# Optimization experiments

Hardware: AMD Instinct MI355X
Metric: run time of the kernel (lower is better)

Reference implementation:

```python
import jax, jax.numpy as jnp
import numpy as np

N = 50000
E = 800000
IN_DIM = 256
HID = 256
OUT_DIM = 2


def setup_inputs() -> dict:
    key = jax.random.key(0)
    ks = jax.random.split(key, 10)
    x = jax.random.normal(ks[0], (N, IN_DIM), dtype=jnp.float32)
    edge_index = jax.random.randint(ks[1], (2, E), 0, N, dtype=jnp.int64)
    # Glorot-ish scaling so activations stay well-conditioned through 4 layers
    def w(k, fan_in, fan_out):
        return jax.random.normal(k, (fan_in, fan_out), dtype=jnp.float32) / jnp.sqrt(jnp.float32(fan_in))
    return {
        "x": x,
        "edge_index": edge_index,
        "W0": w(ks[2], IN_DIM, HID), "b0": jnp.zeros((HID,), jnp.float32),
        "W1": w(ks[3], HID, HID),    "b1": jnp.zeros((HID,), jnp.float32),
        "W2": w(ks[4], HID, HID),    "b2": jnp.zeros((HID,), jnp.float32),
        "W3": w(ks[5], HID, OUT_DIM), "b3": jnp.zeros((OUT_DIM,), jnp.float32),
    }


def _gcn_norm(edge_index, n, dtype):
    # PyG gcn_norm with self-loops: deg over destination, norm = d^-1/2[src]*d^-1/2[dst]
    loops = jnp.arange(n, dtype=edge_index.dtype)
    src = jnp.concatenate([edge_index[0], loops])
    dst = jnp.concatenate([edge_index[1], loops])
    deg = jax.ops.segment_sum(jnp.ones_like(dst, dtype=dtype), dst, num_segments=n)
    dis = deg ** -0.5  # deg >= 1 due to self-loops
    norm = dis[src] * dis[dst]
    return src, dst, norm


def reference(x, edge_index, W0, b0, W1, b1, W2, b2, W3, b3):
    n = x.shape[0]
    src, dst, norm = _gcn_norm(edge_index, n, x.dtype)

    def conv(h, W, b):
        h = h @ W                              # [N, F_out] dense GEMM
        msg = h[src] * norm[:, None]           # edge-gather + scale
        agg = jax.ops.segment_sum(msg, dst, num_segments=n)  # scatter-add
        return agg + b

    h = jax.nn.relu(conv(x, W0, b0))
    h = jax.nn.relu(conv(h, W1, b1))
    h = jax.nn.relu(conv(h, W2, b2))
    return conv(h, W3, b3)
```

## Files before the change

kernel.cpp:

```cpp
#include <hip/hip_runtime.h>

#define N_NODES 50000
#define N_EDGES 800000

static inline int cdiv(int a, int b) { return (a + b - 1) / b; }

typedef __attribute__((ext_vector_type(8))) short bf16x8;
typedef __attribute__((ext_vector_type(4))) float f32x4;

static __device__ __forceinline__ unsigned short f2bf(float f) {
    unsigned int u = __float_as_uint(f);
    unsigned int r = (u + 0x7FFF + ((u >> 16) & 1)) >> 16;
    return (unsigned short)r;
}
static __device__ __forceinline__ float bf2f(unsigned short h) {
    return __uint_as_float((unsigned int)h << 16);
}
static __device__ __forceinline__ float bf_lo(unsigned int u) { return __uint_as_float(u << 16); }
static __device__ __forceinline__ float bf_hi(unsigned int u) { return __uint_as_float(u & 0xFFFF0000u); }


__global__ void k_init_cnt(int* cnt, int n) {
    int i = blockIdx.x * 256 + threadIdx.x;
    if (i < n) cnt[i] = 1;
}

__global__ void k_count(const int* __restrict__ edst, int* cnt, int e) {
    int i = blockIdx.x * 256 + threadIdx.x;
    if (i < e) atomicAdd(&cnt[edst[i]], 1);
}

__global__ __launch_bounds__(256) void k_scan1(const int* __restrict__ cnt,
                                               int* __restrict__ row_ptr,
                                               float* __restrict__ dis,
                                               int* __restrict__ blk, int n) {
    __shared__ int sums[256];
    int t = threadIdx.x;
    int base = blockIdx.x * 1024 + t * 4;
    int c0 = 0, c1 = 0, c2 = 0, c3 = 0;
    if (base + 3 < n) {
        int4 v = *(const int4*)(cnt + base);
        c0 = v.x; c1 = v.y; c2 = v.z; c3 = v.w;
    } else {
        if (base + 0 < n) c0 = cnt[base + 0];
        if (base + 1 < n) c1 = cnt[base + 1];
        if (base + 2 < n) c2 = cnt[base + 2];
        if (base + 3 < n) c3 = cnt[base + 3];
    }
    int s = c0 + c1 + c2 + c3;
    sums[t] = s;
    __syncthreads();
    int x = s;
    for (int off = 1; off < 256; off <<= 1) {
        int y = (t >= off) ? sums[t - off] : 0;
        __syncthreads();
        x += y;
        sums[t] = x;
        __syncthreads();
    }
    int excl = x - s;
    if (base + 0 < n) { row_ptr[base + 0] = excl;                dis[base + 0] = rsqrtf((float)c0); }
    if (base + 1 < n) { row_ptr[base + 1] = excl + c0;           dis[base + 1] = rsqrtf((float)c1); }
    if (base + 2 < n) { row_ptr[base + 2] = excl + c0 + c1;      dis[base + 2] = rsqrtf((float)c2); }
    if (base + 3 < n) { row_ptr[base + 3] = excl + c0 + c1 + c2; dis[base + 3] = rsqrtf((float)c3); }
    if (t == 255) blk[blockIdx.x] = x;
}

__global__ __launch_bounds__(256) void k_scan2(int* __restrict__ blk,
                                               int* __restrict__ row_ptr_n, int nb) {
    __shared__ int sums[256];
    int t = threadIdx.x;
    int s = (t < nb) ? blk[t] : 0;
    sums[t] = s;
    __syncthreads();
    int x = s;
    for (int off = 1; off < 256; off <<= 1) {
        int y = (t >= off) ? sums[t - off] : 0;
        __syncthreads();
        x += y;
        sums[t] = x;
        __syncthreads();
    }
    if (t < nb) blk[t] = x - s;
    if (t == 255) row_ptr_n[0] = x;
}

__global__ __launch_bounds__(256) void k_scan3(int* __restrict__ row_ptr,
                                               int* __restrict__ pos,
                                               const int* __restrict__ blk, int n) {
    int base = blockIdx.x * 1024 + threadIdx.x * 4;
    int off = blk[blockIdx.x];
#pragma unroll
    for (int i = 0; i < 4; ++i) {
        int idx = base + i;
        if (idx < n) {
            int v = row_ptr[idx] + off;
            row_ptr[idx] = v;
            pos[idx] = v;
        }
    }
}

__global__ void k_fill_self(int* pos, const float* __restrict__ dis,
                            int* src_s, float* norm_s, int n) {
    int i = blockIdx.x * 256 + threadIdx.x;
    if (i < n) {
        int p = atomicAdd(&pos[i], 1);
        src_s[p] = i;
        float d = dis[i];
        norm_s[p] = d * d;
    }
}

__global__ void k_fill_edges(const int* __restrict__ esrc, const int* __restrict__ edst,
                             int* pos, const float* __restrict__ dis,
                             int* src_s, float* norm_s, int e) {
    int i = blockIdx.x * 256 + threadIdx.x;
    if (i < e) {
        int s = esrc[i], d = edst[i];
        int p = atomicAdd(&pos[d], 1);
        src_s[p] = s;
        norm_s[p] = dis[s] * dis[d];
    }
}


__global__ __launch_bounds__(256) void k_split_w(const float* __restrict__ W,
                                                 unsigned short* __restrict__ Wth,
                                                 unsigned short* __restrict__ Wtl) {
    int n = blockIdx.x;
    int k = threadIdx.x;
    float v = W[(size_t)k * 256 + n];
    unsigned short h = f2bf(v);
    Wth[(size_t)n * 256 + k] = h;
    Wtl[(size_t)n * 256 + k] = f2bf(v - bf2f(h));
}


__global__ __launch_bounds__(256) void k_split_a(const float* __restrict__ X,
                                                 unsigned short* __restrict__ Xh,
                                                 unsigned short* __restrict__ Xl, long total4) {
    long i = (long)blockIdx.x * 256 + threadIdx.x;
    if (i >= total4) return;
    float4 v = *(const float4*)(X + i * 4);
    ushort4 h, l;
    h.x = f2bf(v.x); l.x = f2bf(v.x - bf2f(h.x));
    h.y = f2bf(v.y); l.y = f2bf(v.y - bf2f(h.y));
    h.z = f2bf(v.z); l.z = f2bf(v.z - bf2f(h.z));
    h.w = f2bf(v.w); l.w = f2bf(v.w - bf2f(h.w));
    *(ushort4*)(Xh + i * 4) = h;
    *(ushort4*)(Xl + i * 4) = l;
}


#define GEMM_RB 196

__global__ __launch_bounds__(256) void k_gemm_mfma(const unsigned short* __restrict__ Ah,
                                                   const unsigned short* __restrict__ Al,
                                                   const unsigned short* __restrict__ Wth,
                                                   const unsigned short* __restrict__ Wtl,
                                                   unsigned short* __restrict__ C, int M) {
    __shared__ unsigned short Wh[64][264];
    __shared__ unsigned short Wl[64][264];
    int rowblk = blockIdx.x % GEMM_RB;
    int colblk = blockIdx.x / GEMM_RB;
    int c0 = colblk * 64;
    int m0 = rowblk * 256;
    int t = threadIdx.x;

    {
        int r = t >> 2;
        int k0 = (t & 3) * 64;
        const unsigned short* gh = Wth + (size_t)(c0 + r) * 256 + k0;
        const unsigned short* gl = Wtl + (size_t)(c0 + r) * 256 + k0;
        unsigned short* lh = &Wh[r][k0];
        unsigned short* ll = &Wl[r][k0];
#pragma unroll
        for (int i = 0; i < 8; ++i) {
            *(uint4*)(lh + i * 8) = *(const uint4*)(gh + i * 8);
            *(uint4*)(ll + i * 8) = *(const uint4*)(gl + i * 8);
        }
    }
    __syncthreads();

    int lane = t & 63, wave = t >> 6;
    int quad = lane >> 4, l16 = lane & 15;

    f32x4 acc[4][4];
#pragma unroll
    for (int i = 0; i < 4; ++i)
#pragma unroll
        for (int j = 0; j < 4; ++j) acc[i][j] = (f32x4){0.f, 0.f, 0.f, 0.f};

    for (int kc = 0; kc < 8; ++kc) {
        int ko = kc * 32 + quad * 8;
        bf16x8 ahf[4], alf[4];
#pragma unroll
        for (int mt = 0; mt < 4; ++mt) {
            int m = m0 + wave * 64 + mt * 16 + l16;
            if (m >= M) m = M - 1;
            ahf[mt] = *(const bf16x8*)(Ah + (size_t)m * 256 + ko);
            alf[mt] = *(const bf16x8*)(Al + (size_t)m * 256 + ko);
        }
#pragma unroll
        for (int nt = 0; nt < 4; ++nt) {
            bf16x8 bh = *(const bf16x8*)&Wh[nt * 16 + l16][ko];
            bf16x8 bl = *(const bf16x8*)&Wl[nt * 16 + l16][ko];
#pragma unroll
            for (int mt = 0; mt < 4; ++mt) {
                acc[mt][nt] = __builtin_amdgcn_mfma_f32_16x16x32_bf16(ahf[mt], bh, acc[mt][nt], 0, 0, 0);
                acc[mt][nt] = __builtin_amdgcn_mfma_f32_16x16x32_bf16(ahf[mt], bl, acc[mt][nt], 0, 0, 0);
                acc[mt][nt] = __builtin_amdgcn_mfma_f32_16x16x32_bf16(alf[mt], bh, acc[mt][nt], 0, 0, 0);
            }
        }
    }

#pragma unroll
    for (int mt = 0; mt < 4; ++mt) {
#pragma unroll
        for (int r = 0; r < 4; ++r) {
            int row = m0 + wave * 64 + mt * 16 + quad * 4 + r;
            if (row < M) {
                unsigned short* cp = C + (size_t)row * 256 + c0 + l16;
#pragma unroll
                for (int nt = 0; nt < 4; ++nt) cp[nt * 16] = f2bf(acc[mt][nt][r]);
            }
        }
    }
}


__global__ __launch_bounds__(256) void k_agg256(const unsigned short* __restrict__ t,
                                                const int* __restrict__ row_ptr,
                                                const int* __restrict__ src_s,
                                                const float* __restrict__ norm_s,
                                                const float* __restrict__ bias,
                                                unsigned short* __restrict__ outh,
                                                unsigned short* __restrict__ outl, int n) {
    int lane = threadIdx.x & 63;
    int wave = threadIdx.x >> 6;
    int node = blockIdx.x * 4 + wave;
    if (node >= n) return;
    int half = lane >> 5;
    int fl = lane & 31;
    int beg = row_ptr[node], end = row_ptr[node + 1];
    float acc[8] = {};
    const unsigned short* tp = t + fl * 8;

    int e = beg + half;
    for (; e + 2 < end; e += 4) {
        int s0 = src_s[e], s1 = src_s[e + 2];
        float w0 = norm_s[e], w1 = norm_s[e + 2];
        uint4 v0 = *(const uint4*)(tp + (size_t)s0 * 256);
        uint4 v1 = *(const uint4*)(tp + (size_t)s1 * 256);
        acc[0] += w0 * bf_lo(v0.x) + w1 * bf_lo(v1.x);
        acc[1] += w0 * bf_hi(v0.x) + w1 * bf_hi(v1.x);
        acc[2] += w0 * bf_lo(v0.y) + w1 * bf_lo(v1.y);
        acc[3] += w0 * bf_hi(v0.y) + w1 * bf_hi(v1.y);
        acc[4] += w0 * bf_lo(v0.z) + w1 * bf_lo(v1.z);
        acc[5] += w0 * bf_hi(v0.z) + w1 * bf_hi(v1.z);
        acc[6] += w0 * bf_lo(v0.w) + w1 * bf_lo(v1.w);
        acc[7] += w0 * bf_hi(v0.w) + w1 * bf_hi(v1.w);
    }
    if (e < end) {
        int s0 = src_s[e];
        float w0 = norm_s[e];
        uint4 v0 = *(const uint4*)(tp + (size_t)s0 * 256);
        acc[0] += w0 * bf_lo(v0.x);
        acc[1] += w0 * bf_hi(v0.x);
        acc[2] += w0 * bf_lo(v0.y);
        acc[3] += w0 * bf_hi(v0.y);
        acc[4] += w0 * bf_lo(v0.z);
        acc[5] += w0 * bf_hi(v0.z);
        acc[6] += w0 * bf_lo(v0.w);
        acc[7] += w0 * bf_hi(v0.w);
    }
#pragma unroll
    for (int i = 0; i < 8; ++i) acc[i] += __shfl_xor(acc[i], 32);

    if (half == 0) {
        const float* bp = bias + fl * 8;
        ushort4 h0, h1, l0, l1;
        float v;
        unsigned short h;
#define EMIT(idx, dst_h, dst_l)                         \
        v = acc[idx] + bp[idx];                         \
        v = v > 0.f ? v : 0.f;                          \
        h = f2bf(v); dst_h = h; dst_l = f2bf(v - bf2f(h));
        EMIT(0, h0.x, l0.x) EMIT(1, h0.y, l0.y) EMIT(2, h0.z, l0.z) EMIT(3, h0.w, l0.w)
        EMIT(4, h1.x, l1.x) EMIT(5, h1.y, l1.y) EMIT(6, h1.z, l1.z) EMIT(7, h1.w, l1.w)
#undef EMIT
        unsigned short* oh = outh + (size_t)node * 256 + fl * 8;
        unsigned short* ol = outl + (size_t)node * 256 + fl * 8;
        *(ushort4*)(oh + 0) = h0;
        *(ushort4*)(oh + 4) = h1;
        *(ushort4*)(ol + 0) = l0;
        *(ushort4*)(ol + 4) = l1;
    }
}


__global__ __launch_bounds__(256) void k_gemm_out2(const unsigned short* __restrict__ Hh,
                                                   const unsigned short* __restrict__ Hl,
                                                   const float* __restrict__ W3,
                                                   float* __restrict__ t2, int n) {
    int lane = threadIdx.x & 63;
    int wave = threadIdx.x >> 6;
    int row = blockIdx.x * 4 + wave;
    if (row >= n) return;
    ushort4 ah = *(const ushort4*)(Hh + (size_t)row * 256 + lane * 4);
    ushort4 al = *(const ushort4*)(Hl + (size_t)row * 256 + lane * 4);
    float4 v;
    v.x = bf2f(ah.x) + bf2f(al.x);
    v.y = bf2f(ah.y) + bf2f(al.y);
    v.z = bf2f(ah.z) + bf2f(al.z);
    v.w = bf2f(ah.w) + bf2f(al.w);
    float4 w01 = *(const float4*)(W3 + lane * 8);
    float4 w23 = *(const float4*)(W3 + lane * 8 + 4);
    float s0 = v.x * w01.x + v.y * w01.z + v.z * w23.x + v.w * w23.z;
    float s1 = v.x * w01.y + v.y * w01.w + v.z * w23.y + v.w * w23.w;
#pragma unroll
    for (int off = 32; off > 0; off >>= 1) {
        s0 += __shfl_down(s0, off);
        s1 += __shfl_down(s1, off);
    }
    if (lane == 0) {
        t2[(size_t)row * 2 + 0] = s0;
        t2[(size_t)row * 2 + 1] = s1;
    }
}

__global__ void k_agg2(const float* __restrict__ t2,
                       const int* __restrict__ row_ptr,
                       const int* __restrict__ src_s,
                       const float* __restrict__ norm_s,
                       const float* __restrict__ b3,
                       float* __restrict__ out, int n) {
    int node = blockIdx.x * 256 + threadIdx.x;
    if (node >= n) return;
    int beg = row_ptr[node], end = row_ptr[node + 1];
    float a0 = 0.f, a1 = 0.f;
    for (int e = beg; e < end; ++e) {
        int s = src_s[e];
        float w = norm_s[e];
        float2 v = *(const float2*)(t2 + (size_t)s * 2);
        a0 += w * v.x;
        a1 += w * v.y;
    }
    out[(size_t)node * 2 + 0] = a0 + b3[0];
    out[(size_t)node * 2 + 1] = a1 + b3[1];
}


extern "C" void kernel_launch(void* const* d_in, const int* in_sizes, int n_in,
                              void* d_out, int out_size, void* d_ws, size_t ws_size,
                              hipStream_t stream) {
    const int N = N_NODES, E = N_EDGES;
    const float* x  = (const float*)d_in[0];
    const int* ei   = (const int*)d_in[1];
    const int* esrc = ei;
    const int* edst = ei + E;
    const float* W0 = (const float*)d_in[2];
    const float* b0 = (const float*)d_in[3];
    const float* W1 = (const float*)d_in[4];
    const float* b1 = (const float*)d_in[5];
    const float* W2 = (const float*)d_in[6];
    const float* b2 = (const float*)d_in[7];
    const float* W3 = (const float*)d_in[8];
    const float* b3 = (const float*)d_in[9];
    float* out = (float*)d_out;

    unsigned short* Ahh = (unsigned short*)d_ws;
    unsigned short* All = Ahh + (size_t)N * 256;
    unsigned short* Tb  = All + (size_t)N * 256;
    unsigned short* Wth = Tb + (size_t)N * 256;
    unsigned short* Wtl = Wth + 256 * 256;
    float* t2     = (float*)(Wtl + 256 * 256);
    float* dis    = t2 + (size_t)N * 2;
    float* norm_s = dis + N;
    int*   cnt    = (int*)(norm_s + (E + N));
    int*   row_ptr= cnt + N;
    int*   pos    = row_ptr + (N + 1);
    int*   src_s  = pos + N;
    int*   blk    = src_s + (E + N);

    const int NB = cdiv(N, 1024);

    k_init_cnt<<<cdiv(N, 256), 256, 0, stream>>>(cnt, N);
    k_count<<<cdiv(E, 256), 256, 0, stream>>>(edst, cnt, E);
    k_scan1<<<NB, 256, 0, stream>>>(cnt, row_ptr, dis, blk, N);
    k_scan2<<<1, 256, 0, stream>>>(blk, row_ptr + N, NB);
    k_scan3<<<NB, 256, 0, stream>>>(row_ptr, pos, blk, N);
    k_fill_self<<<cdiv(N, 256), 256, 0, stream>>>(pos, dis, src_s, norm_s, N);
    k_fill_edges<<<cdiv(E, 256), 256, 0, stream>>>(esrc, edst, pos, dis, src_s, norm_s, E);

    const int ggrid = GEMM_RB * 4;
    const int agrid = cdiv(N, 4);
    const long total4 = (long)N * 64;

    k_split_a<<<cdiv((int)total4, 256), 256, 0, stream>>>(x, Ahh, All, total4);
    k_split_w<<<256, 256, 0, stream>>>(W0, Wth, Wtl);
    k_gemm_mfma<<<ggrid, 256, 0, stream>>>(Ahh, All, Wth, Wtl, Tb, N);
    k_agg256<<<agrid, 256, 0, stream>>>(Tb, row_ptr, src_s, norm_s, b0, Ahh, All, N);
    k_split_w<<<256, 256, 0, stream>>>(W1, Wth, Wtl);
    k_gemm_mfma<<<ggrid, 256, 0, stream>>>(Ahh, All, Wth, Wtl, Tb, N);
    k_agg256<<<agrid, 256, 0, stream>>>(Tb, row_ptr, src_s, norm_s, b1, Ahh, All, N);
    k_split_w<<<256, 256, 0, stream>>>(W2, Wth, Wtl);
    k_gemm_mfma<<<ggrid, 256, 0, stream>>>(Ahh, All, Wth, Wtl, Tb, N);
    k_agg256<<<agrid, 256, 0, stream>>>(Tb, row_ptr, src_s, norm_s, b2, Ahh, All, N);
    k_gemm_out2<<<agrid, 256, 0, stream>>>(Ahh, All, W3, t2, N);
    k_agg2<<<cdiv(N, 256), 256, 0, stream>>>(t2, row_ptr, src_s, norm_s, b3, out, N);
}
```

Measured before the change: 564.8 us.

## Permute hidden feature layout for vector GEMM stores, merge weight-split and fill kernels

The GEMM epilogue now writes four adjacent bf16 outputs as one ushort4 store. To keep this correct, hidden features are stored in a permuted column order, and the weight split, aggregation bias indexing and output GEMM weight indexing are adjusted to match. All three hidden weight splits are merged into one launch with separate buffers, and the self-loop and edge fill kernels are merged into one. Aggregation adds an 8-edge unrolled loop for more memory-level parallelism. The permutation has to stay consistent across layers, and layer 0 keeps the natural input order, which adds index arithmetic.

```diff
diff --git a/kernel.cpp b/kernel.cpp
--- a/kernel.cpp
+++ b/kernel.cpp
@@ -18,6 +18,18 @@
 }
 static __device__ __forceinline__ float bf_lo(unsigned int u) { return __uint_as_float(u << 16); }
 static __device__ __forceinline__ float bf_hi(unsigned int u) { return __uint_as_float(u & 0xFFFF0000u); }
+
+
+static __device__ __forceinline__ void acc8(float* acc, uint4 v, float wgt) {
+    acc[0] += wgt * bf_lo(v.x);
+    acc[1] += wgt * bf_hi(v.x);
+    acc[2] += wgt * bf_lo(v.y);
+    acc[3] += wgt * bf_hi(v.y);
+    acc[4] += wgt * bf_lo(v.z);
+    acc[5] += wgt * bf_hi(v.z);
+    acc[6] += wgt * bf_lo(v.w);
+    acc[7] += wgt * bf_hi(v.w);
+}
 
 
 __global__ void k_init_cnt(int* cnt, int n) {
@@ -101,39 +113,44 @@
     }
 }
 
-__global__ void k_fill_self(int* pos, const float* __restrict__ dis,
-                            int* src_s, float* norm_s, int n) {
-    int i = blockIdx.x * 256 + threadIdx.x;
-    if (i < n) {
-        int p = atomicAdd(&pos[i], 1);
-        src_s[p] = i;
-        float d = dis[i];
-        norm_s[p] = d * d;
-    }
-}
-
-__global__ void k_fill_edges(const int* __restrict__ esrc, const int* __restrict__ edst,
-                             int* pos, const float* __restrict__ dis,
-                             int* src_s, float* norm_s, int e) {
+__global__ void k_fill(const int* __restrict__ esrc, const int* __restrict__ edst,
+                       int* pos, const float* __restrict__ dis,
+                       int* src_s, float* norm_s, int e, int n) {
     int i = blockIdx.x * 256 + threadIdx.x;
     if (i < e) {
         int s = esrc[i], d = edst[i];
         int p = atomicAdd(&pos[d], 1);
         src_s[p] = s;
         norm_s[p] = dis[s] * dis[d];
-    }
-}
-
-
-__global__ __launch_bounds__(256) void k_split_w(const float* __restrict__ W,
-                                                 unsigned short* __restrict__ Wth,
-                                                 unsigned short* __restrict__ Wtl) {
-    int n = blockIdx.x;
-    int k = threadIdx.x;
+    } else if (i < e + n) {
+        int v = i - e;
+        int p = atomicAdd(&pos[v], 1);
+        src_s[p] = v;
+        float d = dis[v];
+        norm_s[p] = d * d;
+    }
+}
+
+
+__global__ __launch_bounds__(256) void k_split_w3(const float* __restrict__ W0,
+                                                  const float* __restrict__ W1,
+                                                  const float* __restrict__ W2,
+                                                  unsigned short* __restrict__ Wth,
+                                                  unsigned short* __restrict__ Wtl) {
+    int layer = blockIdx.x >> 8;
+    int n = blockIdx.x & 255;
+    int p = threadIdx.x;
+    const float* W = layer == 0 ? W0 : (layer == 1 ? W1 : W2);
+    int k = p;
+    if (layer != 0) {
+        int pl = p & 63;
+        k = (p & ~63) + (pl & 3) * 16 + (pl >> 2);
+    }
     float v = W[(size_t)k * 256 + n];
     unsigned short h = f2bf(v);
-    Wth[(size_t)n * 256 + k] = h;
-    Wtl[(size_t)n * 256 + k] = f2bf(v - bf2f(h));
+    size_t o = (size_t)layer * 65536 + (size_t)n * 256 + p;
+    Wth[o] = h;
+    Wtl[o] = f2bf(v - bf2f(h));
 }
 
 
@@ -186,21 +203,30 @@
     int lane = t & 63, wave = t >> 6;
     int quad = lane >> 4, l16 = lane & 15;
 
+    const unsigned short* aph[4];
+    const unsigned short* apl[4];
+#pragma unroll
+    for (int mt = 0; mt < 4; ++mt) {
+        int m = m0 + wave * 64 + mt * 16 + l16;
+        if (m >= M) m = M - 1;
+        aph[mt] = Ah + (size_t)m * 256;
+        apl[mt] = Al + (size_t)m * 256;
+    }
+
     f32x4 acc[4][4];
 #pragma unroll
     for (int i = 0; i < 4; ++i)
 #pragma unroll
         for (int j = 0; j < 4; ++j) acc[i][j] = (f32x4){0.f, 0.f, 0.f, 0.f};
 
+#pragma unroll 2
     for (int kc = 0; kc < 8; ++kc) {
         int ko = kc * 32 + quad * 8;
         bf16x8 ahf[4], alf[4];
 #pragma unroll
         for (int mt = 0; mt < 4; ++mt) {
-            int m = m0 + wave * 64 + mt * 16 + l16;
-            if (m >= M) m = M - 1;
-            ahf[mt] = *(const bf16x8*)(Ah + (size_t)m * 256 + ko);
-            alf[mt] = *(const bf16x8*)(Al + (size_t)m * 256 + ko);
+            ahf[mt] = *(const bf16x8*)(aph[mt] + ko);
+            alf[mt] = *(const bf16x8*)(apl[mt] + ko);
         }
 #pragma unroll
         for (int nt = 0; nt < 4; ++nt) {
@@ -221,9 +247,12 @@
         for (int r = 0; r < 4; ++r) {
             int row = m0 + wave * 64 + mt * 16 + quad * 4 + r;
             if (row < M) {
-                unsigned short* cp = C + (size_t)row * 256 + c0 + l16;
-#pragma unroll
-                for (int nt = 0; nt < 4; ++nt) cp[nt * 16] = f2bf(acc[mt][nt][r]);
+                ushort4 sv;
+                sv.x = f2bf(acc[mt][0][r]);
+                sv.y = f2bf(acc[mt][1][r]);
+                sv.z = f2bf(acc[mt][2][r]);
+                sv.w = f2bf(acc[mt][3][r]);
+                *(ushort4*)(C + (size_t)row * 256 + c0 + l16 * 4) = sv;
             }
         }
     }
@@ -248,48 +277,50 @@
     const unsigned short* tp = t + fl * 8;
 
     int e = beg + half;
+    for (; e + 6 < end; e += 8) {
+        int s0 = src_s[e], s1 = src_s[e + 2], s2 = src_s[e + 4], s3 = src_s[e + 6];
+        float w0 = norm_s[e], w1 = norm_s[e + 2], w2 = norm_s[e + 4], w3 = norm_s[e + 6];
+        uint4 v0 = *(const uint4*)(tp + (size_t)s0 * 256);
+        uint4 v1 = *(const uint4*)(tp + (size_t)s1 * 256);
+        uint4 v2 = *(const uint4*)(tp + (size_t)s2 * 256);
+        uint4 v3 = *(const uint4*)(tp + (size_t)s3 * 256);
+        acc8(acc, v0, w0); acc8(acc, v1, w1); acc8(acc, v2, w2); acc8(acc, v3, w3);
+    }
     for (; e + 2 < end; e += 4) {
         int s0 = src_s[e], s1 = src_s[e + 2];
         float w0 = norm_s[e], w1 = norm_s[e + 2];
         uint4 v0 = *(const uint4*)(tp + (size_t)s0 * 256);
         uint4 v1 = *(const uint4*)(tp + (size_t)s1 * 256);
-        acc[0] += w0 * bf_lo(v0.x) + w1 * bf_lo(v1.x);
-        acc[1] += w0 * bf_hi(v0.x) + w1 * bf_hi(v1.x);
-        acc[2] += w0 * bf_lo(v0.y) + w1 * bf_lo(v1.y);
-        acc[3] += w0 * bf_hi(v0.y) + w1 * bf_hi(v1.y);
-        acc[4] += w0 * bf_lo(v0.z) + w1 * bf_lo(v1.z);
-        acc[5] += w0 * bf_hi(v0.z) + w1 * bf_hi(v1.z);
-        acc[6] += w0 * bf_lo(v0.w) + w1 * bf_lo(v1.w);
-        acc[7] += w0 * bf_hi(v0.w) + w1 * bf_hi(v1.w);
+        acc8(acc, v0, w0); acc8(acc, v1, w1);
     }
     if (e < end) {
         int s0 = src_s[e];
         float w0 = norm_s[e];
         uint4 v0 = *(const uint4*)(tp + (size_t)s0 * 256);
-        acc[0] += w0 * bf_lo(v0.x);
-        acc[1] += w0 * bf_hi(v0.x);
-        acc[2] += w0 * bf_lo(v0.y);
-        acc[3] += w0 * bf_hi(v0.y);
-        acc[4] += w0 * bf_lo(v0.z);
-        acc[5] += w0 * bf_hi(v0.z);
-        acc[6] += w0 * bf_lo(v0.w);
-        acc[7] += w0 * bf_hi(v0.w);
-    }
+        acc8(acc, v0, w0);
+    }
+
 #pragma unroll
     for (int i = 0; i < 8; ++i) acc[i] += __shfl_xor(acc[i], 32);
 
     if (half == 0) {
-        const float* bp = bias + fl * 8;
         ushort4 h0, h1, l0, l1;
-        float v;
-        unsigned short h;
-#define EMIT(idx, dst_h, dst_l)                         \
-        v = acc[idx] + bp[idx];                         \
-        v = v > 0.f ? v : 0.f;                          \
-        h = f2bf(v); dst_h = h; dst_l = f2bf(v - bf2f(h));
-        EMIT(0, h0.x, l0.x) EMIT(1, h0.y, l0.y) EMIT(2, h0.z, l0.z) EMIT(3, h0.w, l0.w)
-        EMIT(4, h1.x, l1.x) EMIT(5, h1.y, l1.y) EMIT(6, h1.z, l1.z) EMIT(7, h1.w, l1.w)
-#undef EMIT
+#pragma unroll
+        for (int j = 0; j < 8; ++j) {
+            int cb = (fl >> 3) * 64 + (j & 3) * 16 + (fl & 7) * 2 + (j >> 2);
+            float v = acc[j] + bias[cb];
+            v = v > 0.f ? v : 0.f;
+            unsigned short h = f2bf(v);
+            unsigned short l = f2bf(v - bf2f(h));
+            if (j == 0) { h0.x = h; l0.x = l; }
+            else if (j == 1) { h0.y = h; l0.y = l; }
+            else if (j == 2) { h0.z = h; l0.z = l; }
+            else if (j == 3) { h0.w = h; l0.w = l; }
+            else if (j == 4) { h1.x = h; l1.x = l; }
+            else if (j == 5) { h1.y = h; l1.y = l; }
+            else if (j == 6) { h1.z = h; l1.z = l; }
+            else { h1.w = h; l1.w = l; }
+        }
         unsigned short* oh = outh + (size_t)node * 256 + fl * 8;
         unsigned short* ol = outl + (size_t)node * 256 + fl * 8;
         *(ushort4*)(oh + 0) = h0;
@@ -310,15 +341,19 @@
     if (row >= n) return;
     ushort4 ah = *(const ushort4*)(Hh + (size_t)row * 256 + lane * 4);
     ushort4 al = *(const ushort4*)(Hl + (size_t)row * 256 + lane * 4);
-    float4 v;
-    v.x = bf2f(ah.x) + bf2f(al.x);
-    v.y = bf2f(ah.y) + bf2f(al.y);
-    v.z = bf2f(ah.z) + bf2f(al.z);
-    v.w = bf2f(ah.w) + bf2f(al.w);
-    float4 w01 = *(const float4*)(W3 + lane * 8);
-    float4 w23 = *(const float4*)(W3 + lane * 8 + 4);
-    float s0 = v.x * w01.x + v.y * w01.z + v.z * w23.x + v.w * w23.z;
-    float s1 = v.x * w01.y + v.y * w01.w + v.z * w23.y + v.w * w23.w;
+    float v[4];
+    v[0] = bf2f(ah.x) + bf2f(al.x);
+    v[1] = bf2f(ah.y) + bf2f(al.y);
+    v[2] = bf2f(ah.z) + bf2f(al.z);
+    v[3] = bf2f(ah.w) + bf2f(al.w);
+    float s0 = 0.f, s1 = 0.f;
+#pragma unroll
+    for (int i = 0; i < 4; ++i) {
+        int c = (lane >> 4) * 64 + i * 16 + (lane & 15);
+        float2 w = *(const float2*)(W3 + (size_t)c * 2);
+        s0 += v[i] * w.x;
+        s1 += v[i] * w.y;
+    }
 #pragma unroll
     for (int off = 32; off > 0; off >>= 1) {
         s0 += __shfl_down(s0, off);
@@ -374,8 +409,8 @@
     unsigned short* All = Ahh + (size_t)N * 256;
     unsigned short* Tb  = All + (size_t)N * 256;
     unsigned short* Wth = Tb + (size_t)N * 256;
-    unsigned short* Wtl = Wth + 256 * 256;
-    float* t2     = (float*)(Wtl + 256 * 256);
+    unsigned short* Wtl = Wth + 3 * 65536;
+    float* t2     = (float*)(Wtl + 3 * 65536);
     float* dis    = t2 + (size_t)N * 2;
     float* norm_s = dis + N;
     int*   cnt    = (int*)(norm_s + (E + N));
@@ -391,22 +426,20 @@
     k_scan1<<<NB, 256, 0, stream>>>(cnt, row_ptr, dis, blk, N);
     k_scan2<<<1, 256, 0, stream>>>(blk, row_ptr + N, NB);
     k_scan3<<<NB, 256, 0, stream>>>(row_ptr, pos, blk, N);
-    k_fill_self<<<cdiv(N, 256), 256, 0, stream>>>(pos, dis, src_s, norm_s, N);
-    k_fill_edges<<<cdiv(E, 256), 256, 0, stream>>>(esrc, edst, pos, dis, src_s, norm_s, E);
+    k_fill<<<cdiv(E + N, 256), 256, 0, stream>>>(esrc, edst, pos, dis, src_s, norm_s, E, N);
 
     const int ggrid = GEMM_RB * 4;
     const int agrid = cdiv(N, 4);
     const long total4 = (long)N * 64;
 
     k_split_a<<<cdiv((int)total4, 256), 256, 0, stream>>>(x, Ahh, All, total4);
-    k_split_w<<<256, 256, 0, stream>>>(W0, Wth, Wtl);
+    k_split_w3<<<768, 256, 0, stream>>>(W0, W1, W2, Wth, Wtl);
+
     k_gemm_mfma<<<ggrid, 256, 0, stream>>>(Ahh, All, Wth, Wtl, Tb, N);
     k_agg256<<<agrid, 256, 0, stream>>>(Tb, row_ptr, src_s, norm_s, b0, Ahh, All, N);
-    k_split_w<<<256, 256, 0, stream>>>(W1, Wth, Wtl);
-    k_gemm_mfma<<<ggrid, 256, 0, stream>>>(Ahh, All, Wth, Wtl, Tb, N);
+    k_gemm_mfma<<<ggrid, 256, 0, stream>>>(Ahh, All, Wth + 65536, Wtl + 65536, Tb, N);
     k_agg256<<<agrid, 256, 0, stream>>>(Tb, row_ptr, src_s, norm_s, b1, Ahh, All, N);
-    k_split_w<<<256, 256, 0, stream>>>(W2, Wth, Wtl);
-    k_gemm_mfma<<<ggrid, 256, 0, stream>>>(Ahh, All, Wth, Wtl, Tb, N);
+    k_gemm_mfma<<<ggrid, 256, 0, stream>>>(Ahh, All, Wth + 2 * 65536, Wtl + 2 * 65536, Tb, N);
     k_agg256<<<agrid, 256, 0, stream>>>(Tb, row_ptr, src_s, norm_s, b2, Ahh, All, N);
     k_gemm_out2<<<agrid, 256, 0, stream>>>(Ahh, All, W3, t2, N);
     k_agg2<<<cdiv(N, 256), 256, 0, stream>>>(t2, row_ptr, src_s, norm_s, b3, out, N);
```

After: 545.3 us. 3.5% less time.
